# Kernel tuning notes

Hardware: AMD Instinct MI355X
Metric: run time of the kernel (lower is better)

Reference implementation:

```python
import jax, jax.numpy as jnp
import numpy as np

N = 100_000
E = 1_000_000
D = 64
NORM_FACTOR = 100.0
LN_EPS = 1e-5


def setup_inputs() -> dict:
    key = jax.random.key(0)
    ks = jax.random.split(key, 8)
    h = jax.random.normal(ks[0], (N, D), dtype=jnp.float32)
    distances = jax.random.uniform(ks[1], (E, 1), dtype=jnp.float32)
    edges = jax.random.randint(ks[2], (2, E), 0, N, dtype=jnp.int64)
    node_mask = jnp.ones((N, 1), dtype=jnp.float32)
    edge_mask = jnp.ones((E, 1), dtype=jnp.float32)
    s = 1.0 / np.sqrt(D)
    W_lin = jax.random.normal(ks[3], (D, D), dtype=jnp.float32) * s
    b_lin = jnp.zeros((D,), dtype=jnp.float32)
    att_W1 = jax.random.normal(ks[4], (D, 2 * D + 1), dtype=jnp.float32) * (1.0 / np.sqrt(2 * D + 1))
    att_b1 = jnp.zeros((D,), dtype=jnp.float32)
    att_W2 = jax.random.normal(ks[5], (1, D), dtype=jnp.float32) * s
    att_b2 = jnp.zeros((1,), dtype=jnp.float32)
    ln_g = jnp.ones((D,), dtype=jnp.float32)
    ln_b = jnp.zeros((D,), dtype=jnp.float32)
    return {"h": h, "distances": distances, "edges": edges, "node_mask": node_mask,
            "edge_mask": edge_mask, "W_lin": W_lin, "b_lin": b_lin,
            "att_W1": att_W1, "att_b1": att_b1, "att_W2": att_W2, "att_b2": att_b2,
            "ln_g": ln_g, "ln_b": ln_b}


def reference(h, distances, edges, node_mask, edge_mask, W_lin, b_lin,
              att_W1, att_b1, att_W2, att_b2, ln_g, ln_b):
    # Linear projection: [N, D]
    x = h @ W_lin.T + b_lin
    row, col = edges[0], edges[1]
    x_row = x[row]          # [E, D]
    x_col = x[col]          # [E, D]
    # DenseAtt: MLP(concat(x_row, x_col, dist)) -> sigmoid -> * edge_mask
    cat = jnp.concatenate([x_row, x_col, distances], axis=1)  # [E, 2D+1]
    hdn = jax.nn.silu(cat @ att_W1.T + att_b1)                # [E, D]
    att = jax.nn.sigmoid(hdn @ att_W2.T + att_b2) * edge_mask # [E, 1]
    # Attention-weighted scatter-sum aggregation into row segments
    agg = x_col * att
    out = jax.ops.segment_sum(agg, row, num_segments=x.shape[0]) / NORM_FACTOR
    out = out + x           # residual
    # LayerNorm + activation
    mu = jnp.mean(out, axis=-1, keepdims=True)
    var = jnp.mean(jnp.square(out - mu), axis=-1, keepdims=True)
    y = (out - mu) * jax.lax.rsqrt(var + LN_EPS) * ln_g + ln_b
    return jax.nn.silu(y)
```

## Files before the change

kernel.cpp:

```cpp
#include <hip/hip_runtime.h>
#include <hip/hip_bf16.h>

#define N_NODES 100000
#define N_EDGES 1000000
#define DIM 64
#define NORM_INV 0.01f
#define LN_EPS 1e-5f
#define N_TILES 6250
#define PROJ_BLOCKS 1563
#define N_BUCKETS 782
#define NB_PAD 800
#define SC_EDGES 4096
#define SC_BLOCKS 245
#define OFS_STRIDE 784
#define L2E 1.4426950408889634f
#define LN2 0.6931471805599453f
#define CAP 2560

typedef __attribute__((ext_vector_type(8))) short short8;
typedef __attribute__((ext_vector_type(4))) float f32x4;

__device__ __forceinline__ unsigned short f2bf(float f) {
    union { float f; unsigned u; } x; x.f = f;
    unsigned r = x.u + 0x7FFFu + ((x.u >> 16) & 1u);
    return (unsigned short)(r >> 16);
}
__device__ __forceinline__ float bf2f(unsigned short s) {
    union { unsigned u; float f; } x; x.u = ((unsigned)s) << 16; return x.f;
}

__global__ __launch_bounds__(256) void prep_frags(
    const float* __restrict__ W, const float* __restrict__ att_W1,
    const float* __restrict__ att_b1, const float* __restrict__ att_W2,
    short8* __restrict__ whi, short8* __restrict__ wlo,
    short8* __restrict__ wa, short8* __restrict__ wb,
    float4* __restrict__ tab) {
    const int l = threadIdx.x & 63;
    const int nt = threadIdx.x >> 6;
    const int c = l & 15, q = l >> 4;
    const int n = nt * 16 + c;
#pragma unroll
    for (int ks = 0; ks < 2; ++ks) {
        const int k0 = ks * 32 + q * 8;
        short8 hi8, lo8, a8, b8;
#pragma unroll
        for (int jj = 0; jj < 8; ++jj) {
            float w = W[n * 64 + k0 + jj];
            unsigned short hh = f2bf(w);
            hi8[jj] = (short)hh;
            lo8[jj] = (short)f2bf(w - bf2f(hh));
            a8[jj] = (short)f2bf(att_W1[n * 129 + k0 + jj]);
            b8[jj] = (short)f2bf(att_W1[n * 129 + 64 + k0 + jj]);
        }
        const int idx = (nt * 2 + ks) * 64 + l;
        whi[idx] = hi8; wlo[idx] = lo8; wa[idx] = a8; wb[idx] = b8;
    }
    if (threadIdx.x < 64) {
        const int f = threadIdx.x;
        tab[f] = make_float4(att_W2[f] * LN2, att_W1[f * 129 + 128] * L2E,
                             att_b1[f] * L2E, 0.f);
    }
}

__global__ __launch_bounds__(256) void proj_scatter(
    const float* __restrict__ h, const float* __restrict__ bl,
    const short8* __restrict__ whi, const short8* __restrict__ wlo,
    const short8* __restrict__ wa, const short8* __restrict__ wb,
    const int* __restrict__ edges, const float* __restrict__ dist,
    const float* __restrict__ emask,
    uint2* __restrict__ srec, int* __restrict__ ofsT,
    unsigned short* __restrict__ xv, unsigned short* __restrict__ u_bf) {
    __shared__ __align__(16) char pool[39168];
    __shared__ int wsum[4];

    if (blockIdx.x >= PROJ_BLOCKS) {
        int* lh = (int*)pool;
        int* lofs = (int*)pool + NB_PAD;
        uint2* lsort = (uint2*)(pool + 6400);
        const int blk = blockIdx.x - PROJ_BLOCKS;
        const int tid = threadIdx.x;
        const int lane = tid & 63;
        const int w = tid >> 6;
        for (int i = tid; i < NB_PAD; i += 256) lh[i] = 0;
        __syncthreads();

        const int eb = blk * SC_EDGES;
        const int total = min(SC_EDGES, N_EDGES - eb);

        int rows[16], rank[16];
        uint2 recs[16];
        const int e0 = eb + tid * 16;
#pragma unroll
        for (int g = 0; g < 4; ++g) {
            const int e = e0 + g * 4;
            if (e + 4 <= N_EDGES) {
                const int4 rr = *(const int4*)(edges + e);
                const int4 cc = *(const int4*)(edges + N_EDGES + e);
                const float4 dd = *(const float4*)(dist + e);
                const float4 mm = *(const float4*)(emask + e);
                rows[g*4+0] = rr.x; rows[g*4+1] = rr.y; rows[g*4+2] = rr.z; rows[g*4+3] = rr.w;
                const int c4[4] = {cc.x, cc.y, cc.z, cc.w};
                const float d4[4] = {dd.x, dd.y, dd.z, dd.w};
                const float m4[4] = {mm.x, mm.y, mm.z, mm.w};
#pragma unroll
                for (int i = 0; i < 4; ++i) {
                    const int ii = g * 4 + i;
                    recs[ii].x = (unsigned)c4[i] | ((unsigned)(rows[ii] & 127) << 24);
                    recs[ii].y = (unsigned)f2bf(d4[i]) |
                                 ((unsigned)f2bf(m4[i] * NORM_INV) << 16);
                    rank[ii] = atomicAdd(&lh[rows[ii] >> 7], 1);
                }
            } else {
#pragma unroll
                for (int i = 0; i < 4; ++i) {
                    const int ii = g * 4 + i;
                    const int ee = e + i;
                    if (ee < N_EDGES) {
                        rows[ii] = edges[ee];
                        recs[ii].x = (unsigned)edges[N_EDGES + ee] |
                                     ((unsigned)(rows[ii] & 127) << 24);
                        recs[ii].y = (unsigned)f2bf(dist[ee]) |
                                     ((unsigned)f2bf(emask[ee] * NORM_INV) << 16);
                        rank[ii] = atomicAdd(&lh[rows[ii] >> 7], 1);
                    } else {
                        rows[ii] = -1;
                    }
                }
            }
        }
        __syncthreads();

        const int b0 = tid * 4;
        int c0 = 0, c1 = 0, c2 = 0, c3 = 0;
        if (b0 < NB_PAD) { c0 = lh[b0]; c1 = lh[b0+1]; c2 = lh[b0+2]; c3 = lh[b0+3]; }
        const int S = c0 + c1 + c2 + c3;
        int sc = S;
#pragma unroll
        for (int off = 1; off < 64; off <<= 1) {
            int u = __shfl_up(sc, off);
            if (lane >= off) sc += u;
        }
        if (lane == 63) wsum[w] = sc;
        __syncthreads();
        int wbase = 0;
        if (w > 0) wbase = wsum[0];
        if (w > 1) wbase += wsum[1];
        if (w > 2) wbase += wsum[2];
        const int excl = sc - S + wbase;
        if (b0 < NB_PAD) {
            lofs[b0] = excl;
            lofs[b0+1] = excl + c0;
            lofs[b0+2] = excl + c0 + c1;
            lofs[b0+3] = excl + c0 + c1 + c2;
        }
        __syncthreads();

#pragma unroll
        for (int i = 0; i < 16; ++i) {
            if (rows[i] >= 0) {
                const int bk = rows[i] >> 7;
                lsort[lofs[bk] + rank[i]] = recs[i];
            }
        }
        __syncthreads();

        for (int s = tid; s < total; s += 256)
            srec[(size_t)blk * SC_EDGES + s] = lsort[s];
        for (int b = tid; b < 783; b += 256)
            ofsT[blk * OFS_STRIDE + b] = lofs[b];
        return;
    }

    const int lane = threadIdx.x & 63;
    const int wv = threadIdx.x >> 6;
    const int c = lane & 15, q = lane >> 4;
    const int tile = blockIdx.x * 4 + wv;
    if (tile >= N_TILES) return;
    const int n0 = tile * 16;

    short8 Whi[4][2], Wlo[4][2], Wa[4][2], Wb[4][2];
    float bias[4];
#pragma unroll
    for (int nt = 0; nt < 4; ++nt) {
        bias[nt] = bl[nt * 16 + c];
#pragma unroll
        for (int ks = 0; ks < 2; ++ks) {
            const int idx = (nt * 2 + ks) * 64 + lane;
            Whi[nt][ks] = whi[idx]; Wlo[nt][ks] = wlo[idx];
            Wa[nt][ks] = wa[idx];   Wb[nt][ks] = wb[idx];
        }
    }

    short8 Ahi[2], Alo[2];
#pragma unroll
    for (int ks = 0; ks < 2; ++ks) {
        const float* hp = h + (size_t)(n0 + c) * 64 + ks * 32 + q * 8;
        f32x4 p0 = *(const f32x4*)hp;
        f32x4 p1 = *(const f32x4*)(hp + 4);
        short8 hi8, lo8;
#pragma unroll
        for (int jj = 0; jj < 4; ++jj) {
            unsigned short hh = f2bf(p0[jj]);
            hi8[jj] = (short)hh; lo8[jj] = (short)f2bf(p0[jj] - bf2f(hh));
            unsigned short h2 = f2bf(p1[jj]);
            hi8[4 + jj] = (short)h2; lo8[4 + jj] = (short)f2bf(p1[jj] - bf2f(h2));
        }
        Ahi[ks] = hi8; Alo[ks] = lo8;
    }

    f32x4 xacc[4] = {{0,0,0,0},{0,0,0,0},{0,0,0,0},{0,0,0,0}};
#pragma unroll
    for (int ks = 0; ks < 2; ++ks)
#pragma unroll
        for (int nt = 0; nt < 4; ++nt) {
            xacc[nt] = __builtin_amdgcn_mfma_f32_16x16x32_bf16(Ahi[ks], Whi[nt][ks], xacc[nt], 0, 0, 0);
            xacc[nt] = __builtin_amdgcn_mfma_f32_16x16x32_bf16(Ahi[ks], Wlo[nt][ks], xacc[nt], 0, 0, 0);
            xacc[nt] = __builtin_amdgcn_mfma_f32_16x16x32_bf16(Alo[ks], Whi[nt][ks], xacc[nt], 0, 0, 0);
        }

    unsigned short* lw = (unsigned short*)pool + wv * (16 * 72);
#pragma unroll
    for (int r = 0; r < 4; ++r) {
        const int node = n0 + q * 4 + r;
        unsigned short xb[4];
#pragma unroll
        for (int nt = 0; nt < 4; ++nt) {
            unsigned short v16 = f2bf(xacc[nt][r] + bias[nt]);
            xb[nt] = v16;
            lw[(q * 4 + r) * 72 + nt * 16 + c] = v16;
        }
        uint2 pk;
        pk.x = (unsigned)xb[0] | ((unsigned)xb[1] << 16);
        pk.y = (unsigned)xb[2] | ((unsigned)xb[3] << 16);
        *(uint2*)(xv + (size_t)node * 128 + c * 8) = pk;
    }

    short8 Ax[2];
#pragma unroll
    for (int ks = 0; ks < 2; ++ks)
        Ax[ks] = *(const short8*)&lw[c * 72 + ks * 32 + q * 8];

    f32x4 uacc[4] = {{0,0,0,0},{0,0,0,0},{0,0,0,0},{0,0,0,0}};
    f32x4 vacc[4] = {{0,0,0,0},{0,0,0,0},{0,0,0,0},{0,0,0,0}};
#pragma unroll
    for (int ks = 0; ks < 2; ++ks)
#pragma unroll
        for (int nt = 0; nt < 4; ++nt) {
            uacc[nt] = __builtin_amdgcn_mfma_f32_16x16x32_bf16(Ax[ks], Wa[nt][ks], uacc[nt], 0, 0, 0);
            vacc[nt] = __builtin_amdgcn_mfma_f32_16x16x32_bf16(Ax[ks], Wb[nt][ks], vacc[nt], 0, 0, 0);
        }
#pragma unroll
    for (int r = 0; r < 4; ++r) {
        const int node = n0 + q * 4 + r;
        uint2 pu;
        pu.x = (unsigned)f2bf(uacc[0][r] * L2E) | ((unsigned)f2bf(uacc[1][r] * L2E) << 16);
        pu.y = (unsigned)f2bf(uacc[2][r] * L2E) | ((unsigned)f2bf(uacc[3][r] * L2E) << 16);
        *(uint2*)(u_bf + (size_t)node * 64 + c * 4) = pu;
        uint2 pk;
        pk.x = (unsigned)f2bf(vacc[0][r] * L2E) | ((unsigned)f2bf(vacc[1][r] * L2E) << 16);
        pk.y = (unsigned)f2bf(vacc[2][r] * L2E) | ((unsigned)f2bf(vacc[3][r] * L2E) << 16);
        *(uint2*)(xv + (size_t)node * 128 + c * 8 + 4) = pk;
    }
}

__global__ __launch_bounds__(512, 4) void agg_fused(
    const uint2* __restrict__ srec, const int* __restrict__ ofsT,
    const unsigned short* __restrict__ xv, const unsigned short* __restrict__ u_bf,
    const float4* __restrict__ tab, const float* __restrict__ att_b2,
    const float* __restrict__ ln_g, const float* __restrict__ ln_b,
    float* __restrict__ out) {
    __shared__ __align__(16) uint2 lrecs[CAP + 16];
    __shared__ int hist[128];
    __shared__ int rst[129];
    __shared__ int cur[128];
    __shared__ int wtot;

    const int b = blockIdx.x;
    const int tid = threadIdx.x;
    const int lane = tid & 63;
    const int wv = tid >> 6;

    if (tid < 128) hist[tid] = 0;
    __syncthreads();

    int st = 0, en = 0;
    if (tid < SC_BLOCKS) {
        st = ofsT[tid * OFS_STRIDE + b];
        en = ofsT[tid * OFS_STRIDE + b + 1];
        const unsigned* sx = (const unsigned*)srec;
        const size_t gb = (size_t)tid * SC_EDGES;
        for (int i = st; i < en; ++i)
            atomicAdd(&hist[sx[2 * (gb + i)] >> 24], 1);
    }
    __syncthreads();

    int c = 0, p = 0, sc = 0;
    if (tid < 128) {
        c = hist[tid];
        p = (c + 3) & ~3;
        sc = p;
#pragma unroll
        for (int off = 1; off < 64; off <<= 1) {
            int u = __shfl_up(sc, off);
            if (lane >= off) sc += u;
        }
        if (tid == 63) wtot = sc;
    }
    __syncthreads();
    if (tid < 128) {
        if (tid >= 64) sc += wtot;
        const int excl = sc - p;
        rst[tid] = excl;
        cur[tid] = excl;
        uint2 z; z.x = 0; z.y = 0;
        for (int i = c; i < p; ++i) lrecs[excl + i] = z;
        if (tid == 127) {
            rst[128] = excl + p;
            for (int i = 0; i < 16; ++i) lrecs[excl + p + i] = z;
        }
    }
    __syncthreads();

    if (tid < SC_BLOCKS) {
        const size_t gb = (size_t)tid * SC_EDGES;
        for (int i = st; i < en; ++i) {
            uint2 rec = srec[gb + i];
            const int lr = (int)(rec.x >> 24);
            rec.x &= 0x00FFFFFFu;
            lrecs[atomicAdd(&cur[lr], 1)] = rec;
        }
    }
    __syncthreads();

    const int j = lane & 15;
    const int sl = lane >> 4;
    const float4 t0 = tab[j], t1 = tab[j + 16], t2 = tab[j + 32], t3 = tab[j + 48];
    const float b2L = att_b2[0] * L2E;
    const float gg = ln_g[lane], bb = ln_b[lane];
    const unsigned* xvu = (const unsigned*)xv;

#pragma unroll 1
    for (int k = 0; k < 16; ++k) {
        const int lrw = wv + 8 * k;
        const int r = b * 128 + lrw;
        if (r >= N_NODES) break;

        const uint2 uu = *(const uint2*)(u_bf + (size_t)r * 64 + j * 4);
        const float base0 = __uint_as_float(uu.x << 16) + t0.z;
        const float base1 = __uint_as_float(uu.x & 0xffff0000u) + t1.z;
        const float base2 = __uint_as_float(uu.y << 16) + t2.z;
        const float base3 = __uint_as_float(uu.y & 0xffff0000u) + t3.z;

        const int s0 = rst[lrw];
        const int e1 = rst[lrw + 1];

        float a0 = 0.f, a1 = 0.f, a2 = 0.f, a3 = 0.f;
        if (e1 > s0) {
            uint2 recA = lrecs[s0 + sl];
            uint4 xvA = *(const uint4*)(xvu + (size_t)recA.x * 64 + j * 4);
            for (int e = s0; e < e1; e += 4) {
                const uint2 recB = lrecs[e + 4 + sl];
                const uint4 xvB = *(const uint4*)(xvu + (size_t)recB.x * 64 + j * 4);

                const float dist = __uint_as_float(recA.y << 16);
                const float emN = __uint_as_float(recA.y & 0xffff0000u);
                const float x0 = __uint_as_float(xvA.x << 16);
                const float x1 = __uint_as_float(xvA.x & 0xffff0000u);
                const float x2 = __uint_as_float(xvA.y << 16);
                const float x3 = __uint_as_float(xvA.y & 0xffff0000u);
                const float v0 = __uint_as_float(xvA.z << 16);
                const float v1 = __uint_as_float(xvA.z & 0xffff0000u);
                const float v2 = __uint_as_float(xvA.w << 16);
                const float v3 = __uint_as_float(xvA.w & 0xffff0000u);
                float pv = 0.f, pre, sg;
                pre = fmaf(dist, t0.y, base0) + v0;
                sg = __builtin_amdgcn_rcpf(1.f + __builtin_amdgcn_exp2f(-pre));
                pv = fmaf(pre * sg, t0.x, pv);
                pre = fmaf(dist, t1.y, base1) + v1;
                sg = __builtin_amdgcn_rcpf(1.f + __builtin_amdgcn_exp2f(-pre));
                pv = fmaf(pre * sg, t1.x, pv);
                pre = fmaf(dist, t2.y, base2) + v2;
                sg = __builtin_amdgcn_rcpf(1.f + __builtin_amdgcn_exp2f(-pre));
                pv = fmaf(pre * sg, t2.x, pv);
                pre = fmaf(dist, t3.y, base3) + v3;
                sg = __builtin_amdgcn_rcpf(1.f + __builtin_amdgcn_exp2f(-pre));
                pv = fmaf(pre * sg, t3.x, pv);
                pv += __shfl_xor(pv, 1); pv += __shfl_xor(pv, 2);
                pv += __shfl_xor(pv, 4); pv += __shfl_xor(pv, 8);
                const float sp = fmaf(pv, L2E, b2L);
                const float att =
                    emN * __builtin_amdgcn_rcpf(1.f + __builtin_amdgcn_exp2f(-sp));
                a0 = fmaf(att, x0, a0); a1 = fmaf(att, x1, a1);
                a2 = fmaf(att, x2, a2); a3 = fmaf(att, x3, a3);
                recA = recB; xvA = xvB;
            }
        }
        a0 += __shfl_xor(a0, 16); a0 += __shfl_xor(a0, 32);
        a1 += __shfl_xor(a1, 16); a1 += __shfl_xor(a1, 32);
        a2 += __shfl_xor(a2, 16); a2 += __shfl_xor(a2, 32);
        a3 += __shfl_xor(a3, 16); a3 += __shfl_xor(a3, 32);

        const uint2 xr = *(const uint2*)(xvu + (size_t)r * 64 + j * 4);
        const float o0 = __uint_as_float(xr.x << 16) + a0;
        const float o1 = __uint_as_float(xr.x & 0xffff0000u) + a1;
        const float o2 = __uint_as_float(xr.y << 16) + a2;
        const float o3 = __uint_as_float(xr.y & 0xffff0000u) + a3;

        float ssum = o0 + o1 + o2 + o3;
        ssum += __shfl_xor(ssum, 1); ssum += __shfl_xor(ssum, 2);
        ssum += __shfl_xor(ssum, 4); ssum += __shfl_xor(ssum, 8);
        const float mu = ssum * (1.f / 64.f);
        const float d0 = o0 - mu, d1 = o1 - mu, d2 = o2 - mu, d3 = o3 - mu;
        float vs = d0 * d0 + d1 * d1 + d2 * d2 + d3 * d3;
        vs += __shfl_xor(vs, 1); vs += __shfl_xor(vs, 2);
        vs += __shfl_xor(vs, 4); vs += __shfl_xor(vs, 8);
        const float rstd = rsqrtf(vs * (1.f / 64.f) + LN_EPS);

        const float dk = (sl == 0) ? d0 : (sl == 1) ? d1 : (sl == 2) ? d2 : d3;
        const float y = fmaf(dk * rstd, gg, bb);
        out[(size_t)r * 64 + lane] =
            y * __builtin_amdgcn_rcpf(1.f + __builtin_amdgcn_exp2f(-y * L2E));
    }
}

extern "C" void kernel_launch(void* const* d_in, const int* in_sizes, int n_in,
                              void* d_out, int out_size, void* d_ws, size_t ws_size,
                              hipStream_t stream) {
    const float* h      = (const float*)d_in[0];
    const float* dist   = (const float*)d_in[1];
    const int*   edges  = (const int*)d_in[2];
    const float* emask  = (const float*)d_in[4];
    const float* W_lin  = (const float*)d_in[5];
    const float* b_lin  = (const float*)d_in[6];
    const float* att_W1 = (const float*)d_in[7];
    const float* att_b1 = (const float*)d_in[8];
    const float* att_W2 = (const float*)d_in[9];
    const float* att_b2 = (const float*)d_in[10];
    const float* ln_g   = (const float*)d_in[11];
    const float* ln_b   = (const float*)d_in[12];
    float* out = (float*)d_out;

    char* ws = (char*)d_ws;
    unsigned short* xv   = (unsigned short*)ws;
    unsigned short* u_bf = (unsigned short*)(ws + 25600000);
    uint2* srec          = (uint2*)(ws + 38400000);
    int* ofsT            = (int*)(ws + 46428160);
    float4* tab          = (float4*)(ws + 47196480);
    short8* whi          = (short8*)(ws + 47197504);
    short8* wlo          = (short8*)(ws + 47205696);
    short8* wa           = (short8*)(ws + 47213888);
    short8* wb           = (short8*)(ws + 47222080);

    prep_frags<<<1, 256, 0, stream>>>(W_lin, att_W1, att_b1, att_W2,
                                      whi, wlo, wa, wb, tab);
    proj_scatter<<<PROJ_BLOCKS + SC_BLOCKS, 256, 0, stream>>>(
        h, b_lin, whi, wlo, wa, wb, edges, dist, emask, srec, ofsT, xv, u_bf);
    agg_fused<<<N_BUCKETS, 512, 0, stream>>>(srec, ofsT, xv, u_bf,
                                             tab, att_b2, ln_g, ln_b, out);
}
```

Before: 211.5 us.

## Stage projection weights in LDS and flatten per-bucket record gather across threads

The projection kernel now loads the four bf16 weight fragment sets once per block into shared memory and reads them per MFMA, instead of holding them all in registers. Out-of-range tiles stay alive so the block barriers stay uniform. In the aggregation kernel, the histogram and scatter of bucket records are flattened: a prefix sum over the per-source-block segment lengths lets all 512 threads pull records with a binary search, rather than 245 threads each walking a variable-length segment serially. The goal is less register pressure in the projection and better load balance and memory parallelism in the bucket gather, at the cost of extra LDS traffic, barriers and per-element binary searches.

```diff
diff --git a/kernel.cpp b/kernel.cpp
--- a/kernel.cpp
+++ b/kernel.cpp
@@ -171,25 +171,34 @@
         return;
     }
 
-    const int lane = threadIdx.x & 63;
-    const int wv = threadIdx.x >> 6;
+    const int tid = threadIdx.x;
+    {
+        uint4* l4 = (uint4*)pool;
+        const uint4* g0 = (const uint4*)whi;
+        const uint4* g1 = (const uint4*)wlo;
+        const uint4* g2 = (const uint4*)wa;
+        const uint4* g3 = (const uint4*)wb;
+        l4[tid]        = g0[tid];       l4[256 + tid]  = g0[256 + tid];
+        l4[512 + tid]  = g1[tid];       l4[768 + tid]  = g1[256 + tid];
+        l4[1024 + tid] = g2[tid];       l4[1280 + tid] = g2[256 + tid];
+        l4[1536 + tid] = g3[tid];       l4[1792 + tid] = g3[256 + tid];
+    }
+    __syncthreads();
+    const short8* Lwhi = (const short8*)pool;
+    const short8* Lwlo = Lwhi + 512;
+    const short8* Lwa  = Lwhi + 1024;
+    const short8* Lwb  = Lwhi + 1536;
+
+    const int lane = tid & 63;
+    const int wv = tid >> 6;
     const int c = lane & 15, q = lane >> 4;
     const int tile = blockIdx.x * 4 + wv;
-    if (tile >= N_TILES) return;
-    const int n0 = tile * 16;
-
-    short8 Whi[4][2], Wlo[4][2], Wa[4][2], Wb[4][2];
+    const bool valid = (tile < N_TILES);
+    const int n0 = valid ? tile * 16 : 0;
+
     float bias[4];
 #pragma unroll
-    for (int nt = 0; nt < 4; ++nt) {
-        bias[nt] = bl[nt * 16 + c];
-#pragma unroll
-        for (int ks = 0; ks < 2; ++ks) {
-            const int idx = (nt * 2 + ks) * 64 + lane;
-            Whi[nt][ks] = whi[idx]; Wlo[nt][ks] = wlo[idx];
-            Wa[nt][ks] = wa[idx];   Wb[nt][ks] = wb[idx];
-        }
-    }
+    for (int nt = 0; nt < 4; ++nt) bias[nt] = bl[nt * 16 + c];
 
     short8 Ahi[2], Alo[2];
 #pragma unroll
@@ -213,10 +222,14 @@
     for (int ks = 0; ks < 2; ++ks)
 #pragma unroll
         for (int nt = 0; nt < 4; ++nt) {
-            xacc[nt] = __builtin_amdgcn_mfma_f32_16x16x32_bf16(Ahi[ks], Whi[nt][ks], xacc[nt], 0, 0, 0);
-            xacc[nt] = __builtin_amdgcn_mfma_f32_16x16x32_bf16(Ahi[ks], Wlo[nt][ks], xacc[nt], 0, 0, 0);
-            xacc[nt] = __builtin_amdgcn_mfma_f32_16x16x32_bf16(Alo[ks], Whi[nt][ks], xacc[nt], 0, 0, 0);
-        }
+            const short8 fhi = Lwhi[(nt * 2 + ks) * 64 + lane];
+            const short8 flo = Lwlo[(nt * 2 + ks) * 64 + lane];
+            xacc[nt] = __builtin_amdgcn_mfma_f32_16x16x32_bf16(Ahi[ks], fhi, xacc[nt], 0, 0, 0);
+            xacc[nt] = __builtin_amdgcn_mfma_f32_16x16x32_bf16(Ahi[ks], flo, xacc[nt], 0, 0, 0);
+            xacc[nt] = __builtin_amdgcn_mfma_f32_16x16x32_bf16(Alo[ks], fhi, xacc[nt], 0, 0, 0);
+        }
+
+    __syncthreads();
 
     unsigned short* lw = (unsigned short*)pool + wv * (16 * 72);
 #pragma unroll
@@ -229,10 +242,12 @@
             xb[nt] = v16;
             lw[(q * 4 + r) * 72 + nt * 16 + c] = v16;
         }
-        uint2 pk;
-        pk.x = (unsigned)xb[0] | ((unsigned)xb[1] << 16);
-        pk.y = (unsigned)xb[2] | ((unsigned)xb[3] << 16);
-        *(uint2*)(xv + (size_t)node * 128 + c * 8) = pk;
+        if (valid) {
+            uint2 pk;
+            pk.x = (unsigned)xb[0] | ((unsigned)xb[1] << 16);
+            pk.y = (unsigned)xb[2] | ((unsigned)xb[3] << 16);
+            *(uint2*)(xv + (size_t)node * 128 + c * 8) = pk;
+        }
     }
 
     short8 Ax[2];
@@ -246,20 +261,24 @@
     for (int ks = 0; ks < 2; ++ks)
 #pragma unroll
         for (int nt = 0; nt < 4; ++nt) {
-            uacc[nt] = __builtin_amdgcn_mfma_f32_16x16x32_bf16(Ax[ks], Wa[nt][ks], uacc[nt], 0, 0, 0);
-            vacc[nt] = __builtin_amdgcn_mfma_f32_16x16x32_bf16(Ax[ks], Wb[nt][ks], vacc[nt], 0, 0, 0);
-        }
-#pragma unroll
-    for (int r = 0; r < 4; ++r) {
-        const int node = n0 + q * 4 + r;
-        uint2 pu;
-        pu.x = (unsigned)f2bf(uacc[0][r] * L2E) | ((unsigned)f2bf(uacc[1][r] * L2E) << 16);
-        pu.y = (unsigned)f2bf(uacc[2][r] * L2E) | ((unsigned)f2bf(uacc[3][r] * L2E) << 16);
-        *(uint2*)(u_bf + (size_t)node * 64 + c * 4) = pu;
-        uint2 pk;
-        pk.x = (unsigned)f2bf(vacc[0][r] * L2E) | ((unsigned)f2bf(vacc[1][r] * L2E) << 16);
-        pk.y = (unsigned)f2bf(vacc[2][r] * L2E) | ((unsigned)f2bf(vacc[3][r] * L2E) << 16);
-        *(uint2*)(xv + (size_t)node * 128 + c * 8 + 4) = pk;
+            const short8 fa = Lwa[(nt * 2 + ks) * 64 + lane];
+            const short8 fb = Lwb[(nt * 2 + ks) * 64 + lane];
+            uacc[nt] = __builtin_amdgcn_mfma_f32_16x16x32_bf16(Ax[ks], fa, uacc[nt], 0, 0, 0);
+            vacc[nt] = __builtin_amdgcn_mfma_f32_16x16x32_bf16(Ax[ks], fb, vacc[nt], 0, 0, 0);
+        }
+    if (valid) {
+#pragma unroll
+        for (int r = 0; r < 4; ++r) {
+            const int node = n0 + q * 4 + r;
+            uint2 pu;
+            pu.x = (unsigned)f2bf(uacc[0][r] * L2E) | ((unsigned)f2bf(uacc[1][r] * L2E) << 16);
+            pu.y = (unsigned)f2bf(uacc[2][r] * L2E) | ((unsigned)f2bf(uacc[3][r] * L2E) << 16);
+            *(uint2*)(u_bf + (size_t)node * 64 + c * 4) = pu;
+            uint2 pk;
+            pk.x = (unsigned)f2bf(vacc[0][r] * L2E) | ((unsigned)f2bf(vacc[1][r] * L2E) << 16);
+            pk.y = (unsigned)f2bf(vacc[2][r] * L2E) | ((unsigned)f2bf(vacc[3][r] * L2E) << 16);
+            *(uint2*)(xv + (size_t)node * 128 + c * 8 + 4) = pk;
+        }
     }
 }
 
@@ -273,6 +292,9 @@
     __shared__ int hist[128];
     __shared__ int rst[129];
     __shared__ int cur[128];
+    __shared__ int sst[256];
+    __shared__ int dbase[257];
+    __shared__ int wsum4[4];
     __shared__ int wtot;
 
     const int b = blockIdx.x;
@@ -281,16 +303,43 @@
     const int wv = tid >> 6;
 
     if (tid < 128) hist[tid] = 0;
-    __syncthreads();
-
-    int st = 0, en = 0;
-    if (tid < SC_BLOCKS) {
-        st = ofsT[tid * OFS_STRIDE + b];
-        en = ofsT[tid * OFS_STRIDE + b + 1];
-        const unsigned* sx = (const unsigned*)srec;
-        const size_t gb = (size_t)tid * SC_EDGES;
-        for (int i = st; i < en; ++i)
-            atomicAdd(&hist[sx[2 * (gb + i)] >> 24], 1);
+
+    int stv = 0, len = 0, sc0 = 0;
+    if (tid < 256) {
+        if (tid < SC_BLOCKS) {
+            stv = ofsT[tid * OFS_STRIDE + b];
+            len = ofsT[tid * OFS_STRIDE + b + 1] - stv;
+        }
+        sst[tid] = stv;
+        sc0 = len;
+#pragma unroll
+        for (int off = 1; off < 64; off <<= 1) {
+            int u = __shfl_up(sc0, off);
+            if (lane >= off) sc0 += u;
+        }
+        if (lane == 63) wsum4[wv] = sc0;
+    }
+    __syncthreads();
+    if (tid < 256) {
+        int wbase = 0;
+        if (wv > 0) wbase = wsum4[0];
+        if (wv > 1) wbase += wsum4[1];
+        if (wv > 2) wbase += wsum4[2];
+        dbase[tid] = wbase + sc0 - len;
+        if (tid == 255) dbase[256] = wbase + sc0;
+    }
+    __syncthreads();
+    const int cnt = dbase[245];
+
+    for (int m = tid; m < cnt; m += 512) {
+        int lo = 0, hi = 245;
+        while (hi - lo > 1) {
+            const int mid = (lo + hi) >> 1;
+            if (dbase[mid] <= m) lo = mid; else hi = mid;
+        }
+        const unsigned key =
+            ((const unsigned*)srec)[2 * ((size_t)lo * SC_EDGES + sst[lo] + (m - dbase[lo]))];
+        atomicAdd(&hist[key >> 24], 1);
     }
     __syncthreads();
 
@@ -321,14 +370,16 @@
     }
     __syncthreads();
 
-    if (tid < SC_BLOCKS) {
-        const size_t gb = (size_t)tid * SC_EDGES;
-        for (int i = st; i < en; ++i) {
-            uint2 rec = srec[gb + i];
-            const int lr = (int)(rec.x >> 24);
-            rec.x &= 0x00FFFFFFu;
-            lrecs[atomicAdd(&cur[lr], 1)] = rec;
-        }
+    for (int m = tid; m < cnt; m += 512) {
+        int lo = 0, hi = 245;
+        while (hi - lo > 1) {
+            const int mid = (lo + hi) >> 1;
+            if (dbase[mid] <= m) lo = mid; else hi = mid;
+        }
+        uint2 rec = srec[(size_t)lo * SC_EDGES + sst[lo] + (m - dbase[lo])];
+        const int lr = (int)(rec.x >> 24);
+        rec.x &= 0x00FFFFFFu;
+        lrecs[atomicAdd(&cur[lr], 1)] = rec;
     }
     __syncthreads();
 
```

After: 201.0 us. 5.0% less time.
